# Kernel tuning notes

Hardware: AMD Instinct MI355X
Metric: run time of the kernel (lower is better)

Reference implementation:

```python
import jax, jax.numpy as jnp
import numpy as np

B, N, DEG = 16, 64, 16          # batch, nodes, out-degree per node
IN_F, EDGE_F, OUT_F, H = 1024, 128, 512, 8
F = OUT_F // H                   # n_hidden = 64 (is_concat=True)
E = N * DEG                      # num_edges = 1024
SLOPE = 0.2                      # leaky relu negative slope


def setup_inputs() -> dict:
    key = jax.random.key(0)
    k0, k1, k2, k3, k4 = jax.random.split(key, 5)
    h = jax.random.normal(k0, (B, N, IN_F), dtype=jnp.float32)
    edge_attr = jax.random.normal(k1, (B, E, EDGE_F), dtype=jnp.float32)
    # deterministic adjacency: node i -> nodes (i+k) % N, k=0..DEG-1
    # (includes self-loop, so every softmax row has >=1 neighbor)
    adj = np.zeros((N, N), dtype=np.float32)
    for i in range(N):
        for k in range(DEG):
            adj[i, (i + k) % N] = 1.0
    adj_mat = jnp.asarray(np.broadcast_to(adj, (B, N, N)).copy())
    W_node = jax.random.normal(k2, (IN_F, H * F), dtype=jnp.float32) * 0.03
    W_edge = jax.random.normal(k3, (EDGE_F, H * F), dtype=jnp.float32) * 0.05
    w_attn = jax.random.normal(k4, (3 * F,), dtype=jnp.float32) * 0.1
    return {"h": h, "adj_mat": adj_mat, "edge_attr": edge_attr,
            "W_node": W_node, "W_edge": W_edge, "w_attn": w_attn}


def reference(h, adj_mat, edge_attr, W_node, W_edge, w_attn):
    # node / edge projections
    g = (h @ W_node).reshape(B, N, H, F)                  # [B,N,H,F]
    e_proj = (edge_attr @ W_edge).reshape(B, E, H, F)     # [B,E,H,F]
    # pad edge rows up to N*N (mirrors torch.cat with zero pad)
    e_proj = jnp.pad(e_proj, ((0, 0), (0, N * N - E), (0, 0), (0, 0)))
    # scatter edge features to flattened nonzero adjacency positions,
    # in row-major nonzero order == rank via exclusive cumsum
    idx = adj_mat.reshape(B, N * N).astype(jnp.int32)     # [B,N*N] of 0/1
    rank = jnp.cumsum(idx, axis=1) - idx                  # position among nonzeros
    ef = jnp.take_along_axis(e_proj, rank[:, :, None, None], axis=1)
    ef = ef * idx[:, :, None, None].astype(g.dtype)       # zero where no edge
    ef = ef.reshape(B, N, N, H, F)                        # [B,i,j,H,F]
    # attn(cat[g_i, g_j, edge]) == g_i.w1 + g_j.w2 + edge.w3
    w_i, w_j, w_e = w_attn[:F], w_attn[F:2 * F], w_attn[2 * F:]
    s_i = jnp.einsum('bnhf,f->bnh', g, w_i)
    s_j = jnp.einsum('bnhf,f->bnh', g, w_j)
    s_e = jnp.einsum('bijhf,f->bijh', ef, w_e)
    e = jax.nn.leaky_relu(s_i[:, :, None, :] + s_j[:, None, :, :] + s_e, SLOPE)
    e = jnp.where(adj_mat[..., None] > 0, e, -jnp.inf)    # mask non-edges
    a = jax.nn.softmax(e, axis=2)                         # softmax over j
    # dropout is identity in eval mode
    out = jnp.einsum('bijh,bjhf->bihf', a, g)             # weighted aggregation
    return out.reshape(B, N, H * F)                       # is_concat=True
```

## Files before the change

kernel.cpp:

```cpp
#include <hip/hip_runtime.h>
#include <hip/hip_bf16.h>
#include <stdint.h>

#define SLOPE 0.2f

typedef short s16x8 __attribute__((ext_vector_type(8)));
typedef float f32x4 __attribute__((ext_vector_type(4)));

__device__ __forceinline__ uint32_t pk_bf16(float lo, float hi) {
    uint32_t r;
    asm("v_cvt_pk_bf16_f32 %0, %1, %2" : "=v"(r) : "v"(lo), "v"(hi));
    return r;
}

__global__ __launch_bounds__(256)
void main_kernel(const float* __restrict__ hmat,
                 const float* __restrict__ adj,
                 const float* __restrict__ edge_attr,
                 const float* __restrict__ W_node,
                 const float* __restrict__ W_edge,
                 const float* __restrict__ w_attn,
                 float* __restrict__ g,
                 float* __restrict__ s_e,
                 float* __restrict__ s_i,
                 float* __restrict__ s_j,
                 int* __restrict__ row_start)
{
    __shared__ __align__(16) char U[10240];
    unsigned short* Bs = (unsigned short*)U;
    float* wvs = (float*)U;

    int bx = blockIdx.x, tid = threadIdx.x;

    if (bx < 128) {
        int head = bx & 7, mt = bx >> 3;
        int n0 = head * 64, m0 = mt * 64;
        int wave = tid >> 6, lane = tid & 63;
        int l15 = lane & 15, quad = lane >> 4;
        int wv16 = wave * 16;

        int kp = tid >> 4, nq = tid & 15;

        const float* aFrag  = hmat + (size_t)(m0 + wv16 + l15) * 1024 + quad * 8;
        const float* bpBase = W_node + (size_t)(2 * kp) * 512 + n0 + nq * 4;

        f32x4 acc[4];
        #pragma unroll
        for (int i = 0; i < 4; ++i) acc[i] = (f32x4){0.f, 0.f, 0.f, 0.f};

        float4 a0 = *(const float4*)(aFrag);
        float4 a1 = *(const float4*)(aFrag + 4);
        float4 b0 = *(const float4*)(bpBase);
        float4 b1 = *(const float4*)(bpBase + 512);
        {
            *(uint32_t*)&Bs[(nq * 4 + 0) * 40 + 2 * kp] = pk_bf16(b0.x, b1.x);
            *(uint32_t*)&Bs[(nq * 4 + 1) * 40 + 2 * kp] = pk_bf16(b0.y, b1.y);
            *(uint32_t*)&Bs[(nq * 4 + 2) * 40 + 2 * kp] = pk_bf16(b0.z, b1.z);
            *(uint32_t*)&Bs[(nq * 4 + 3) * 40 + 2 * kp] = pk_bf16(b0.w, b1.w);
        }

        for (int it = 0; it < 32; ++it) {
            union { s16x8 v; uint32_t w[4]; } A;
            A.w[0] = pk_bf16(a0.x, a0.y);
            A.w[1] = pk_bf16(a0.z, a0.w);
            A.w[2] = pk_bf16(a1.x, a1.y);
            A.w[3] = pk_bf16(a1.z, a1.w);

            __syncthreads();

            if (it + 1 < 32) {
                const float* ap = aFrag + (it + 1) * 32;
                a0 = *(const float4*)ap;
                a1 = *(const float4*)(ap + 4);
                const float* bp = bpBase + (size_t)(it + 1) * 32 * 512;
                b0 = *(const float4*)bp;
                b1 = *(const float4*)(bp + 512);
            }
            int cur = it & 1;
            s16x8 af = A.v;
            #pragma unroll
            for (int nt = 0; nt < 4; ++nt) {
                s16x8 bf = *(const s16x8*)&Bs[(cur * 64 + nt * 16 + l15) * 40 + quad * 8];
                acc[nt] = __builtin_amdgcn_mfma_f32_16x16x32_bf16(af, bf, acc[nt], 0, 0, 0);
            }
            if (it + 1 < 32) {
                int nxt = cur ^ 1;
                *(uint32_t*)&Bs[(nxt * 64 + nq * 4 + 0) * 40 + 2 * kp] = pk_bf16(b0.x, b1.x);
                *(uint32_t*)&Bs[(nxt * 64 + nq * 4 + 1) * 40 + 2 * kp] = pk_bf16(b0.y, b1.y);
                *(uint32_t*)&Bs[(nxt * 64 + nq * 4 + 2) * 40 + 2 * kp] = pk_bf16(b0.z, b1.z);
                *(uint32_t*)&Bs[(nxt * 64 + nq * 4 + 3) * 40 + 2 * kp] = pk_bf16(b0.w, b1.w);
            }
        }

        float wi[4], wj[4];
        #pragma unroll
        for (int nt = 0; nt < 4; ++nt) {
            wi[nt] = w_attn[nt * 16 + l15];
            wj[nt] = w_attn[64 + nt * 16 + l15];
        }
        float pi[4], pj[4];
        #pragma unroll
        for (int reg = 0; reg < 4; ++reg) { pi[reg] = 0.f; pj[reg] = 0.f; }
        #pragma unroll
        for (int nt = 0; nt < 4; ++nt) {
            #pragma unroll
            for (int reg = 0; reg < 4; ++reg) {
                int gm = m0 + wv16 + quad * 4 + reg;
                int gn = n0 + nt * 16 + l15;
                g[(size_t)gm * 512 + gn] = acc[nt][reg];
                pi[reg] += acc[nt][reg] * wi[nt];
                pj[reg] += acc[nt][reg] * wj[nt];
            }
        }
        #pragma unroll
        for (int mask = 1; mask < 16; mask <<= 1) {
            #pragma unroll
            for (int reg = 0; reg < 4; ++reg) {
                pi[reg] += __shfl_xor(pi[reg], mask);
                pj[reg] += __shfl_xor(pj[reg], mask);
            }
        }
        if (l15 == 0) {
            #pragma unroll
            for (int reg = 0; reg < 4; ++reg) {
                int r = m0 + wv16 + quad * 4 + reg;
                s_i[(size_t)r * 8 + head] = pi[reg];
                s_j[(size_t)r * 8 + head] = pj[reg];
            }
        }
    } else if (bx < 256) {
        {
            int c = tid & 127, halfT = tid >> 7;
            const float* we = w_attn + 128;
            #pragma unroll
            for (int hh = 0; hh < 4; ++hh) {
                int h = halfT * 4 + hh;
                float s = 0.f;
                const float* row = W_edge + (size_t)c * 512 + h * 64;
                #pragma unroll 8
                for (int f = 0; f < 64; ++f) s += row[f] * we[f];
                wvs[c * 8 + h] = s;
            }
        }
        __syncthreads();
        int e = (bx - 128) * 128 + (tid >> 1);
        int half = tid & 1;
        const float4* erow = (const float4*)(edge_attr + (size_t)e * 128 + half * 64);
        f32x4 accl = {0.f, 0.f, 0.f, 0.f};
        f32x4 acch = {0.f, 0.f, 0.f, 0.f};
        for (int c4 = 0; c4 < 16; ++c4) {
            float4 v = erow[c4];
            #pragma unroll
            for (int u = 0; u < 4; ++u) {
                int c = half * 64 + c4 * 4 + u;
                f32x4 w0 = *(const f32x4*)&wvs[c * 8];
                f32x4 w1 = *(const f32x4*)&wvs[c * 8 + 4];
                float x = (u == 0) ? v.x : (u == 1) ? v.y : (u == 2) ? v.z : v.w;
                accl += x * w0;
                acch += x * w1;
            }
        }
        #pragma unroll
        for (int q = 0; q < 4; ++q) {
            accl[q] += __shfl_xor(accl[q], 1);
            acch[q] += __shfl_xor(acch[q], 1);
        }
        if (half == 0) {
            *(f32x4*)(s_e + (size_t)e * 8)     = accl;
            *(f32x4*)(s_e + (size_t)e * 8 + 4) = acch;
        }
    } else {
        int b = bx - 256;
        if (tid < 64) {
            const float* row = adj + (size_t)b * 4096 + (size_t)tid * 64;
            int cnt = 0;
            #pragma unroll 8
            for (int j = 0; j < 64; ++j) cnt += (row[j] > 0.5f) ? 1 : 0;
            int inc = cnt;
            #pragma unroll
            for (int d = 1; d < 64; d <<= 1) {
                int u = __shfl_up(inc, d, 64);
                if (tid >= d) inc += u;
            }
            row_start[b * 64 + tid] = inc - cnt;
        }
    }
}

__global__ __launch_bounds__(256)
void attn_kernel(const float* __restrict__ g,
                 const float* __restrict__ adj,
                 const float* __restrict__ s_e,
                 const float* __restrict__ s_i,
                 const float* __restrict__ s_j,
                 const int*   __restrict__ row_start,
                 float* __restrict__ out)
{
    __shared__ float a_s[16][8];
    __shared__ int nbr[16];
    __shared__ int m_nb_s;

    int bi = blockIdx.x;
    int b = bi >> 6, i = bi & 63;
    int tid = threadIdx.x;

    if (tid < 16) nbr[tid] = 0;
    if (tid < 64) {
        float av = adj[(size_t)b * 4096 + (size_t)i * 64 + tid];
        unsigned long long m = __ballot(av > 0.5f);
        if (av > 0.5f) {
            int before = __popcll(m & ((1ull << tid) - 1ull));
            if (before < 16) nbr[before] = tid;
        }
        if (tid == 0) {
            int c = __popcll(m);
            m_nb_s = (c > 16) ? 16 : c;
        }
    }
    __syncthreads();

    int m_nb = m_nb_s;

    int c0 = tid * 2;
    int h = tid >> 5;
    float2 gv[16];
    #pragma unroll
    for (int k = 0; k < 16; ++k) {
        gv[k] = *(const float2*)(g + (size_t)(b * 64 + nbr[k]) * 512 + c0);
    }

    if (tid < 128) {
        int hh = tid >> 4, k = tid & 15;
        float v;
        if (k < m_nb) {
            int rs = row_start[bi];
            float se = s_e[(size_t)(b * 1024 + rs + k) * 8 + hh];
            float sj = s_j[(size_t)(b * 64 + nbr[k]) * 8 + hh];
            float si = s_i[(size_t)bi * 8 + hh];
            v = si + sj + se;
            v = (v >= 0.f) ? v : SLOPE * v;
        } else {
            v = -1e30f;
        }
        float mx = v;
        #pragma unroll
        for (int mask = 1; mask < 16; mask <<= 1)
            mx = fmaxf(mx, __shfl_xor(mx, mask));
        float e = (k < m_nb) ? __expf(v - mx) : 0.f;
        float ssum = e;
        #pragma unroll
        for (int mask = 1; mask < 16; mask <<= 1)
            ssum += __shfl_xor(ssum, mask);
        a_s[k][hh] = e / ssum;
    }
    __syncthreads();

    float o0 = 0.f, o1 = 0.f;
    #pragma unroll
    for (int k = 0; k < 16; ++k) {
        float ak = a_s[k][h];
        o0 += ak * gv[k].x;
        o1 += ak * gv[k].y;
    }
    out[(size_t)bi * 512 + c0]     = o0;
    out[(size_t)bi * 512 + c0 + 1] = o1;
}

extern "C" void kernel_launch(void* const* d_in, const int* in_sizes, int n_in,
                              void* d_out, int out_size, void* d_ws, size_t ws_size,
                              hipStream_t stream) {
    const float* h_in      = (const float*)d_in[0];
    const float* adj_mat   = (const float*)d_in[1];
    const float* edge_attr = (const float*)d_in[2];
    const float* W_node    = (const float*)d_in[3];
    const float* W_edge    = (const float*)d_in[4];
    const float* w_attn    = (const float*)d_in[5];
    float* out = (float*)d_out;

    char* ws = (char*)d_ws;
    float* g         = (float*)(ws + 0x000000);
    float* s_e       = (float*)(ws + 0x200000);
    float* s_i       = (float*)(ws + 0x280000);
    float* s_j       = (float*)(ws + 0x288000);
    int*   row_start = (int*)  (ws + 0x290000);

    main_kernel<<<272, 256, 0, stream>>>(h_in, adj_mat, edge_attr,
                                         W_node, W_edge, w_attn,
                                         g, s_e, s_i, s_j, row_start);
    attn_kernel<<<1024, 256, 0, stream>>>(g, adj_mat, s_e, s_i, s_j,
                                          row_start, out);
}
```

Measured before the change: 91.72 us.

## Double K-step per iteration with two-deep W_node prefetch in node GEMM

The node-projection GEMM loop now processes 64 K elements per iteration (two MFMA groups) instead of 32, halving the number of __syncthreads barriers. W_node tiles are prefetched two iterations ahead into registers, and the LDS buffer is doubled to hold two K-slices per stage. This targets global-load latency and barrier overhead in the main GEMM, at the cost of more registers and LDS, which may lower occupancy.

After: 87.48 us (median of 2 runs). 4.6% less time.

```diff
diff --git a/kernel.cpp b/kernel.cpp
--- a/kernel.cpp
+++ b/kernel.cpp
@@ -26,7 +26,7 @@
                  float* __restrict__ s_j,
                  int* __restrict__ row_start)
 {
-    __shared__ __align__(16) char U[10240];
+    __shared__ __align__(16) char U[20480];
     unsigned short* Bs = (unsigned short*)U;
     float* wvs = (float*)U;
 
@@ -48,49 +48,89 @@
         #pragma unroll
         for (int i = 0; i < 4; ++i) acc[i] = (f32x4){0.f, 0.f, 0.f, 0.f};
 
-        float4 a0 = *(const float4*)(aFrag);
-        float4 a1 = *(const float4*)(aFrag + 4);
-        float4 b0 = *(const float4*)(bpBase);
-        float4 b1 = *(const float4*)(bpBase + 512);
+        float4 a0, a1, a2, a3;
+        float4 b00, b01, b10, b11;
+
+        b00 = *(const float4*)(bpBase);
+        b01 = *(const float4*)(bpBase + 512);
+        b10 = *(const float4*)(bpBase + 32 * 512);
+        b11 = *(const float4*)(bpBase + 33 * 512);
         {
-            *(uint32_t*)&Bs[(nq * 4 + 0) * 40 + 2 * kp] = pk_bf16(b0.x, b1.x);
-            *(uint32_t*)&Bs[(nq * 4 + 1) * 40 + 2 * kp] = pk_bf16(b0.y, b1.y);
-            *(uint32_t*)&Bs[(nq * 4 + 2) * 40 + 2 * kp] = pk_bf16(b0.z, b1.z);
-            *(uint32_t*)&Bs[(nq * 4 + 3) * 40 + 2 * kp] = pk_bf16(b0.w, b1.w);
-        }
-
-        for (int it = 0; it < 32; ++it) {
-            union { s16x8 v; uint32_t w[4]; } A;
-            A.w[0] = pk_bf16(a0.x, a0.y);
-            A.w[1] = pk_bf16(a0.z, a0.w);
-            A.w[2] = pk_bf16(a1.x, a1.y);
-            A.w[3] = pk_bf16(a1.z, a1.w);
-
-            __syncthreads();
-
-            if (it + 1 < 32) {
-                const float* ap = aFrag + (it + 1) * 32;
-                a0 = *(const float4*)ap;
-                a1 = *(const float4*)(ap + 4);
-                const float* bp = bpBase + (size_t)(it + 1) * 32 * 512;
-                b0 = *(const float4*)bp;
-                b1 = *(const float4*)(bp + 512);
-            }
-            int cur = it & 1;
-            s16x8 af = A.v;
-            #pragma unroll
-            for (int nt = 0; nt < 4; ++nt) {
-                s16x8 bf = *(const s16x8*)&Bs[(cur * 64 + nt * 16 + l15) * 40 + quad * 8];
-                acc[nt] = __builtin_amdgcn_mfma_f32_16x16x32_bf16(af, bf, acc[nt], 0, 0, 0);
-            }
-            if (it + 1 < 32) {
-                int nxt = cur ^ 1;
-                *(uint32_t*)&Bs[(nxt * 64 + nq * 4 + 0) * 40 + 2 * kp] = pk_bf16(b0.x, b1.x);
-                *(uint32_t*)&Bs[(nxt * 64 + nq * 4 + 1) * 40 + 2 * kp] = pk_bf16(b0.y, b1.y);
-                *(uint32_t*)&Bs[(nxt * 64 + nq * 4 + 2) * 40 + 2 * kp] = pk_bf16(b0.z, b1.z);
-                *(uint32_t*)&Bs[(nxt * 64 + nq * 4 + 3) * 40 + 2 * kp] = pk_bf16(b0.w, b1.w);
-            }
-        }
+            const float* q0 = &b00.x; const float* q1 = &b01.x;
+            const float* q2 = &b10.x; const float* q3 = &b11.x;
+            #pragma unroll
+            for (int u = 0; u < 4; ++u) {
+                *(uint32_t*)&Bs[(0 * 64 + nq * 4 + u) * 40 + 2 * kp] = pk_bf16(q0[u], q1[u]);
+                *(uint32_t*)&Bs[(1 * 64 + nq * 4 + u) * 40 + 2 * kp] = pk_bf16(q2[u], q3[u]);
+            }
+        }
+        {
+            const float* bp = bpBase + (size_t)64 * 512;
+            b00 = *(const float4*)bp;
+            b01 = *(const float4*)(bp + 512);
+            b10 = *(const float4*)(bp + 32 * 512);
+            b11 = *(const float4*)(bp + 33 * 512);
+        }
+        a0 = *(const float4*)(aFrag);
+        a1 = *(const float4*)(aFrag + 4);
+        a2 = *(const float4*)(aFrag + 32);
+        a3 = *(const float4*)(aFrag + 36);
+        __syncthreads();
+
+        #define GITER(IT, BUF, NOT_LAST, HAS_PF2)                              \
+        {                                                                      \
+            union { s16x8 v; uint32_t w[4]; } A0, A1;                          \
+            A0.w[0] = pk_bf16(a0.x, a0.y); A0.w[1] = pk_bf16(a0.z, a0.w);      \
+            A0.w[2] = pk_bf16(a1.x, a1.y); A0.w[3] = pk_bf16(a1.z, a1.w);      \
+            A1.w[0] = pk_bf16(a2.x, a2.y); A1.w[1] = pk_bf16(a2.z, a2.w);      \
+            A1.w[2] = pk_bf16(a3.x, a3.y); A1.w[3] = pk_bf16(a3.z, a3.w);      \
+            if (NOT_LAST) {                                                    \
+                const float* ap = aFrag + ((IT) + 1) * 64;                     \
+                a0 = *(const float4*)ap;        a1 = *(const float4*)(ap + 4); \
+                a2 = *(const float4*)(ap + 32); a3 = *(const float4*)(ap + 36);\
+            }                                                                  \
+            {                                                                  \
+                s16x8 af = A0.v;                                               \
+                _Pragma("unroll")                                              \
+                for (int nt = 0; nt < 4; ++nt) {                               \
+                    s16x8 bf = *(const s16x8*)&Bs[(((BUF)*2 + 0) * 64 + nt * 16 + l15) * 40 + quad * 8]; \
+                    acc[nt] = __builtin_amdgcn_mfma_f32_16x16x32_bf16(af, bf, acc[nt], 0, 0, 0); \
+                }                                                              \
+            }                                                                  \
+            {                                                                  \
+                s16x8 af = A1.v;                                               \
+                _Pragma("unroll")                                              \
+                for (int nt = 0; nt < 4; ++nt) {                               \
+                    s16x8 bf = *(const s16x8*)&Bs[(((BUF)*2 + 1) * 64 + nt * 16 + l15) * 40 + quad * 8]; \
+                    acc[nt] = __builtin_amdgcn_mfma_f32_16x16x32_bf16(af, bf, acc[nt], 0, 0, 0); \
+                }                                                              \
+            }                                                                  \
+            if (NOT_LAST) {   \
+                int sb = ((BUF) ^ 1) * 2;                                      \
+                const float* q0 = &b00.x; const float* q1 = &b01.x;            \
+                const float* q2 = &b10.x; const float* q3 = &b11.x;            \
+                _Pragma("unroll")                                              \
+                for (int u = 0; u < 4; ++u) {                                  \
+                    *(uint32_t*)&Bs[((sb + 0) * 64 + nq * 4 + u) * 40 + 2 * kp] = pk_bf16(q0[u], q1[u]); \
+                    *(uint32_t*)&Bs[((sb + 1) * 64 + nq * 4 + u) * 40 + 2 * kp] = pk_bf16(q2[u], q3[u]); \
+                }                                                              \
+            }                                                                  \
+            if (HAS_PF2) {                            \
+                const float* bp = bpBase + (size_t)(((IT) + 2) * 64) * 512;    \
+                b00 = *(const float4*)bp;                                      \
+                b01 = *(const float4*)(bp + 512);                              \
+                b10 = *(const float4*)(bp + 32 * 512);                         \
+                b11 = *(const float4*)(bp + 33 * 512);                         \
+            }                                                                  \
+            if (NOT_LAST) __syncthreads();                                     \
+        }
+
+        for (int ii = 0; ii < 8; ++ii) {
+            int it = 2 * ii;
+            GITER(it,     0, true,           it + 2 < 16);
+            GITER(it + 1, 1, it + 1 < 15,    it + 3 < 16);
+        }
+        #undef GITER
 
         float wi[4], wj[4];
         #pragma unroll
```

## Deepen GEMM K-step to 128 with register prefetch and fold row-scan blocks

Applied to the files above, without the earlier changes.

The node-projection GEMM now handles four 32-wide K chunks per iteration: eight iterations instead of 32, with one barrier each. B tiles are staged two iterations ahead and A one ahead, using double-buffered shared memory of four chunks per buffer. The goal is to cut barrier count and hide global-load latency better. The adjacency row-start scan moves into the first 16 edge-score blocks, dropping 16 extra blocks from the launch. In exchange, register pressure rises (16 float4 staging registers) and shared memory grows to 40KB, which may reduce occupancy.

New measurement: 88.08 us. 4.0% less time.

```diff
diff --git a/kernel.cpp b/kernel.cpp
--- a/kernel.cpp
+++ b/kernel.cpp
@@ -26,7 +26,7 @@
                  float* __restrict__ s_j,
                  int* __restrict__ row_start)
 {
-    __shared__ __align__(16) char U[10240];
+    __shared__ __align__(16) char U[40960];
     unsigned short* Bs = (unsigned short*)U;
     float* wvs = (float*)U;
 
@@ -48,48 +48,92 @@
         #pragma unroll
         for (int i = 0; i < 4; ++i) acc[i] = (f32x4){0.f, 0.f, 0.f, 0.f};
 
-        float4 a0 = *(const float4*)(aFrag);
-        float4 a1 = *(const float4*)(aFrag + 4);
-        float4 b0 = *(const float4*)(bpBase);
-        float4 b1 = *(const float4*)(bpBase + 512);
+        float4 a0, a1, a2, a3, a4, a5, a6, a7;
+        float4 b0, b1, b2, b3, b4, b5, b6, b7;
+
         {
-            *(uint32_t*)&Bs[(nq * 4 + 0) * 40 + 2 * kp] = pk_bf16(b0.x, b1.x);
-            *(uint32_t*)&Bs[(nq * 4 + 1) * 40 + 2 * kp] = pk_bf16(b0.y, b1.y);
-            *(uint32_t*)&Bs[(nq * 4 + 2) * 40 + 2 * kp] = pk_bf16(b0.z, b1.z);
-            *(uint32_t*)&Bs[(nq * 4 + 3) * 40 + 2 * kp] = pk_bf16(b0.w, b1.w);
-        }
-
-        for (int it = 0; it < 32; ++it) {
-            union { s16x8 v; uint32_t w[4]; } A;
-            A.w[0] = pk_bf16(a0.x, a0.y);
-            A.w[1] = pk_bf16(a0.z, a0.w);
-            A.w[2] = pk_bf16(a1.x, a1.y);
-            A.w[3] = pk_bf16(a1.z, a1.w);
-
-            __syncthreads();
-
-            if (it + 1 < 32) {
-                const float* ap = aFrag + (it + 1) * 32;
-                a0 = *(const float4*)ap;
-                a1 = *(const float4*)(ap + 4);
-                const float* bp = bpBase + (size_t)(it + 1) * 32 * 512;
-                b0 = *(const float4*)bp;
-                b1 = *(const float4*)(bp + 512);
-            }
-            int cur = it & 1;
-            s16x8 af = A.v;
-            #pragma unroll
-            for (int nt = 0; nt < 4; ++nt) {
-                s16x8 bf = *(const s16x8*)&Bs[(cur * 64 + nt * 16 + l15) * 40 + quad * 8];
-                acc[nt] = __builtin_amdgcn_mfma_f32_16x16x32_bf16(af, bf, acc[nt], 0, 0, 0);
-            }
-            if (it + 1 < 32) {
-                int nxt = cur ^ 1;
-                *(uint32_t*)&Bs[(nxt * 64 + nq * 4 + 0) * 40 + 2 * kp] = pk_bf16(b0.x, b1.x);
-                *(uint32_t*)&Bs[(nxt * 64 + nq * 4 + 1) * 40 + 2 * kp] = pk_bf16(b0.y, b1.y);
-                *(uint32_t*)&Bs[(nxt * 64 + nq * 4 + 2) * 40 + 2 * kp] = pk_bf16(b0.z, b1.z);
-                *(uint32_t*)&Bs[(nxt * 64 + nq * 4 + 3) * 40 + 2 * kp] = pk_bf16(b0.w, b1.w);
-            }
+            float4 t0, t1;
+            #define STAGE0(C, OFF)                                             \
+            {                                                                  \
+                t0 = *(const float4*)(bpBase + (size_t)(OFF) * 512);           \
+                t1 = *(const float4*)(bpBase + (size_t)(OFF) * 512 + 512);     \
+                const float* q0 = &t0.x; const float* q1 = &t1.x;              \
+                _Pragma("unroll")                                              \
+                for (int u = 0; u < 4; ++u)                                    \
+                    *(uint32_t*)&Bs[((C) * 64 + nq * 4 + u) * 40 + 2 * kp] =   \
+                        pk_bf16(q0[u], q1[u]);                                 \
+            }
+            STAGE0(0, 0); STAGE0(1, 32); STAGE0(2, 64); STAGE0(3, 96);
+            #undef STAGE0
+        }
+        {
+            const float* bp = bpBase + (size_t)128 * 512;
+            b0 = *(const float4*)(bp);             b1 = *(const float4*)(bp + 512);
+            b2 = *(const float4*)(bp + 32 * 512);  b3 = *(const float4*)(bp + 33 * 512);
+            b4 = *(const float4*)(bp + 64 * 512);  b5 = *(const float4*)(bp + 65 * 512);
+            b6 = *(const float4*)(bp + 96 * 512);  b7 = *(const float4*)(bp + 97 * 512);
+        }
+        a0 = *(const float4*)(aFrag);       a1 = *(const float4*)(aFrag + 4);
+        a2 = *(const float4*)(aFrag + 32);  a3 = *(const float4*)(aFrag + 36);
+        a4 = *(const float4*)(aFrag + 64);  a5 = *(const float4*)(aFrag + 68);
+        a6 = *(const float4*)(aFrag + 96);  a7 = *(const float4*)(aFrag + 100);
+        __syncthreads();
+
+        for (int it = 0; it < 8; ++it) {
+            int buf = it & 1;
+            int sbase = buf * 4;
+
+            union { s16x8 v; uint32_t w[4]; } A0, A1, A2, A3;
+            A0.w[0] = pk_bf16(a0.x, a0.y); A0.w[1] = pk_bf16(a0.z, a0.w);
+            A0.w[2] = pk_bf16(a1.x, a1.y); A0.w[3] = pk_bf16(a1.z, a1.w);
+            A1.w[0] = pk_bf16(a2.x, a2.y); A1.w[1] = pk_bf16(a2.z, a2.w);
+            A1.w[2] = pk_bf16(a3.x, a3.y); A1.w[3] = pk_bf16(a3.z, a3.w);
+            A2.w[0] = pk_bf16(a4.x, a4.y); A2.w[1] = pk_bf16(a4.z, a4.w);
+            A2.w[2] = pk_bf16(a5.x, a5.y); A2.w[3] = pk_bf16(a5.z, a5.w);
+            A3.w[0] = pk_bf16(a6.x, a6.y); A3.w[1] = pk_bf16(a6.z, a6.w);
+            A3.w[2] = pk_bf16(a7.x, a7.y); A3.w[3] = pk_bf16(a7.z, a7.w);
+
+            if (it < 7) {
+                const float* ap = aFrag + (size_t)(it + 1) * 128;
+                a0 = *(const float4*)(ap);       a1 = *(const float4*)(ap + 4);
+                a2 = *(const float4*)(ap + 32);  a3 = *(const float4*)(ap + 36);
+                a4 = *(const float4*)(ap + 64);  a5 = *(const float4*)(ap + 68);
+                a6 = *(const float4*)(ap + 96);  a7 = *(const float4*)(ap + 100);
+            }
+
+            #define CHUNK(C, AU)                                               \
+            {                                                                  \
+                s16x8 af = AU.v;                                               \
+                _Pragma("unroll")                                              \
+                for (int nt = 0; nt < 4; ++nt) {                               \
+                    s16x8 bf = *(const s16x8*)&Bs[((sbase + (C)) * 64 + nt * 16 + l15) * 40 + quad * 8]; \
+                    acc[nt] = __builtin_amdgcn_mfma_f32_16x16x32_bf16(af, bf, acc[nt], 0, 0, 0); \
+                }                                                              \
+            }
+            CHUNK(0, A0); CHUNK(1, A1); CHUNK(2, A2); CHUNK(3, A3);
+            #undef CHUNK
+
+            if (it < 7) {
+                int sb = (buf ^ 1) * 4;
+                #define STG(C, BL, BH)                                         \
+                {                                                              \
+                    const float* q0 = &BL.x; const float* q1 = &BH.x;          \
+                    _Pragma("unroll")                                          \
+                    for (int u = 0; u < 4; ++u)                                \
+                        *(uint32_t*)&Bs[((sb + (C)) * 64 + nq * 4 + u) * 40 + 2 * kp] = \
+                            pk_bf16(q0[u], q1[u]);                             \
+                }
+                STG(0, b0, b1); STG(1, b2, b3); STG(2, b4, b5); STG(3, b6, b7);
+                #undef STG
+            }
+            if (it + 2 < 8) {
+                const float* bp = bpBase + (size_t)((it + 2) * 128) * 512;
+                b0 = *(const float4*)(bp);             b1 = *(const float4*)(bp + 512);
+                b2 = *(const float4*)(bp + 32 * 512);  b3 = *(const float4*)(bp + 33 * 512);
+                b4 = *(const float4*)(bp + 64 * 512);  b5 = *(const float4*)(bp + 65 * 512);
+                b6 = *(const float4*)(bp + 96 * 512);  b7 = *(const float4*)(bp + 97 * 512);
+            }
+            if (it < 7) __syncthreads();
         }
 
         float wi[4], wj[4];
@@ -128,7 +172,7 @@
                 s_j[(size_t)r * 8 + head] = pj[reg];
             }
         }
-    } else if (bx < 256) {
+    } else {
         {
             int c = tid & 127, halfT = tid >> 7;
             const float* we = w_attn + 128;
@@ -169,9 +213,8 @@
             *(f32x4*)(s_e + (size_t)e * 8)     = accl;
             *(f32x4*)(s_e + (size_t)e * 8 + 4) = acch;
         }
-    } else {
-        int b = bx - 256;
-        if (tid < 64) {
+        if (bx < 144 && tid < 64) {
+            int b = bx - 128;
             const float* row = adj + (size_t)b * 4096 + (size_t)tid * 64;
             int cnt = 0;
             #pragma unroll 8
@@ -284,7 +327,7 @@
     float* s_j       = (float*)(ws + 0x288000);
     int*   row_start = (int*)  (ws + 0x290000);
 
-    main_kernel<<<272, 256, 0, stream>>>(h_in, adj_mat, edge_attr,
+    main_kernel<<<256, 256, 0, stream>>>(h_in, adj_mat, edge_attr,
                                          W_node, W_edge, w_attn,
                                          g, s_e, s_i, s_j, row_start);
     attn_kernel<<<1024, 256, 0, stream>>>(g, adj_mat, s_e, s_i, s_j,
```
